# Optimization experiments

Hardware: AMD Instinct MI355X
Metric: run time of the kernel (lower is better)

## Reference

```python
import jax, jax.numpy as jnp
import numpy as np

H, HP, NH_M, NH_D = 1024, 64, 8, 8
B, T = 2, 2048
SPARSITY = 8
N_ROT = 32  # int(0.5 * HP), even
BASE = 10000.0


def _rope(x, pos, n_rot, base):
    # x: (..., L, d); pos: broadcastable to (..., L). Rotates first n_rot dims.
    half = n_rot // 2
    inv = base ** (-jnp.arange(half, dtype=x.dtype) / half)  # (half,)
    ang = pos[..., None] * inv                               # (..., L, half)
    cos, sin = jnp.cos(ang), jnp.sin(ang)
    x1, x2 = x[..., :half], x[..., half:n_rot]
    rot = jnp.concatenate([x1 * cos - x2 * sin, x1 * sin + x2 * cos], axis=-1)
    return jnp.concatenate([rot, x[..., n_rot:]], axis=-1)


def setup_inputs() -> dict:
    key = jax.random.key(0)
    ks = jax.random.split(key, 6)
    s = 0.02
    return {
        "X": jax.random.normal(ks[0], (B, T, H), jnp.float32),
        "mosa_router_w": jax.random.normal(ks[1], (H, NH_M), jnp.float32) * s,
        "mosa_wqkv": jax.random.normal(ks[2], (H, NH_M, 3 * HP), jnp.float32) * s,
        "mosa_wo": jax.random.normal(ks[3], (NH_M * HP, H), jnp.float32) * s,
        "dense_wqkv": jax.random.normal(ks[4], (H, NH_D, 3 * HP), jnp.float32) * s,
        "dense_wo": jax.random.normal(ks[5], (NH_D * HP, H), jnp.float32) * s,
    }


def _mosa_branch(X, router_w, wqkv, wo):
    # Expert-choice sparse attention: each head routes its own top-k tokens.
    b, t, _ = X.shape
    k = t // SPARSITY
    scores = jnp.einsum('bth,hn->bnt', X, router_w)                      # (b,nh,T)
    _, idx = jax.lax.top_k(scores, k)                                    # (b,nh,k)
    idx = jnp.sort(idx, axis=-1)                                         # keep temporal order
    gates = jax.nn.sigmoid(jnp.take_along_axis(scores, idx, axis=-1))    # (b,nh,k)
    Xg = jnp.take_along_axis(X[:, None], idx[..., None], axis=2)         # (b,nh,k,h)
    qkv = jnp.einsum('bnkh,hnd->bnkd', Xg, wqkv)                         # (b,nh,k,3hp)
    Q, K, V = jnp.split(qkv, 3, axis=-1)
    pos = idx.astype(X.dtype)                                            # original positions for RoPE
    Q = _rope(Q, pos, N_ROT, BASE)
    K = _rope(K, pos, N_ROT, BASE)
    att = jnp.einsum('bnqd,bnkd->bnqk', Q, K) / jnp.sqrt(jnp.asarray(HP, X.dtype))
    causal = idx[..., :, None] >= idx[..., None, :]                      # causality by original index
    att = jnp.where(causal, att, -jnp.inf)
    AV = jnp.einsum('bnqk,bnkd->bnqd', jax.nn.softmax(att, axis=-1), V)
    AV = AV * gates[..., None]
    # scatter selected-token outputs back to full sequence
    out = jnp.zeros((b, NH_M, t, HP), X.dtype)
    bi = jnp.arange(b)[:, None, None]
    hi = jnp.arange(NH_M)[None, :, None]
    out = out.at[bi, hi, idx].set(AV)                                    # (b,nh,T,hp)
    out = out.transpose(0, 2, 1, 3).reshape(b, t, NH_M * HP)
    return out @ wo


def _dense_branch(X, wqkv, wo):
    b, t, _ = X.shape
    qkv = jnp.einsum('bth,hnd->bntd', X, wqkv)                           # (b,nh,T,3hp)
    Q, K, V = jnp.split(qkv, 3, axis=-1)
    pos = jnp.arange(t, dtype=X.dtype)
    Q = _rope(Q, pos, N_ROT, BASE)
    K = _rope(K, pos, N_ROT, BASE)
    att = jnp.einsum('bnqd,bnkd->bnqk', Q, K) / jnp.sqrt(jnp.asarray(HP, X.dtype))
    causal = jnp.tril(jnp.ones((t, t), bool))
    att = jnp.where(causal, att, -jnp.inf)
    AV = jnp.einsum('bnqk,bnkd->bnqd', jax.nn.softmax(att, axis=-1), V)  # (b,nh,T,hp)
    return AV.transpose(0, 2, 1, 3).reshape(b, t, NH_D * HP) @ wo


def reference(X, mosa_router_w, mosa_wqkv, mosa_wo, dense_wqkv, dense_wo):
    return (_mosa_branch(X, mosa_router_w, mosa_wqkv, mosa_wo)
            + _dense_branch(X, dense_wqkv, dense_wo))
```

## Files before the change

kernel.cpp:

```cpp
#include <hip/hip_runtime.h>
#include <math.h>

constexpr int BB = 2;
constexpr int SEQ = 2048;
constexpr int HD = 1024;
constexpr int DH = 64;
constexpr int NHEAD = 8;
constexpr int D3 = 192;
constexpr int KSEL = 256;
constexpr float NEG = -1e30f;

typedef short short8 __attribute__((ext_vector_type(8)));
typedef float f32x4 __attribute__((ext_vector_type(4)));

__device__ __forceinline__ ushort bf16u(float f) {
  union { float f; unsigned u; } v; v.f = f;
  unsigned r = (v.u + 0x7FFFu + ((v.u >> 16) & 1u)) >> 16;
  return (ushort)r;
}
__device__ __forceinline__ float bf2f(ushort h) {
  union { unsigned u; float f; } v; v.u = ((unsigned)h) << 16;
  return v.f;
}

__device__ __forceinline__ void gl_lds16(const ushort* g, ushort* l) {
  __builtin_amdgcn_global_load_lds(
      (const __attribute__((address_space(1))) unsigned int*)g,
      (__attribute__((address_space(3))) unsigned int*)l, 16, 0, 0);
}

__device__ __forceinline__ unsigned long long rankkey(float s, int idx) {
  union { float f; unsigned u; } v; v.f = s;
  unsigned o = (v.u & 0x80000000u) ? ~v.u : (v.u | 0x80000000u);
  return ((unsigned long long)o << 11) | (unsigned)(2047 - idx);
}

__global__ void cast_bf16x4(const float* __restrict__ x, ushort* __restrict__ y, int n4) {
  int i = blockIdx.x * 256 + threadIdx.x;
  if (i >= n4) return;
  float4 v = ((const float4*)x)[i];
  ushort4 r; r.x = bf16u(v.x); r.y = bf16u(v.y); r.z = bf16u(v.z); r.w = bf16u(v.w);
  ((ushort4*)y)[i] = r;
}

__global__ __launch_bounds__(256) void transpose_cast2(
    const float* __restrict__ W1, ushort* __restrict__ T1,
    const float* __restrict__ W2, ushort* __restrict__ T2, int K, int N) {
  const float* W = blockIdx.z ? W2 : W1;
  ushort* Wt = blockIdx.z ? T2 : T1;
  __shared__ float tile[32][33];
  int n0 = blockIdx.x * 32, k0 = blockIdx.y * 32;
  int tx = threadIdx.x & 31, ty = threadIdx.x >> 5;
#pragma unroll
  for (int i = 0; i < 4; i++)
    tile[ty + 8 * i][tx] = W[(size_t)(k0 + ty + 8 * i) * N + n0 + tx];
  __syncthreads();
#pragma unroll
  for (int i = 0; i < 4; i++)
    Wt[(size_t)(n0 + ty + 8 * i) * K + k0 + tx] = bf16u(tile[tx][ty + 8 * i]);
}

__global__ __launch_bounds__(256) void router2(const float* __restrict__ X,
    const float* __restrict__ rw, float* __restrict__ scores) {
  __shared__ float rwT[8][8][132];
  int tid = threadIdx.x;
  for (int idx = tid; idx < 8192; idx += 256) {
    int h = idx & 1023, n = idx >> 10;
    rwT[n][h >> 7][h & 127] = rw[h * 8 + n];
  }
  __syncthreads();
  int row = blockIdx.x * 32 + (tid >> 3);
  int seg = tid & 7;
  const float* xrow = X + (size_t)row * HD + seg * 128;
  float acc[8] = {};
#pragma unroll 8
  for (int it = 0; it < 32; it++) {
    float4 xv = *(const float4*)(xrow + 4 * it);
#pragma unroll
    for (int n = 0; n < 8; n++) {
      float4 rv = *(const float4*)&rwT[n][seg][4 * it];
      acc[n] += xv.x * rv.x + xv.y * rv.y + xv.z * rv.z + xv.w * rv.w;
    }
  }
#pragma unroll
  for (int n = 0; n < 8; n++) {
    acc[n] += __shfl_xor(acc[n], 1);
    acc[n] += __shfl_xor(acc[n], 2);
    acc[n] += __shfl_xor(acc[n], 4);
  }
  int b = row >> 11, t2 = row & (SEQ - 1);
  scores[((size_t)b * NHEAD + seg) * SEQ + t2] = acc[seg];
}

__global__ __launch_bounds__(256) void topk_partial(const float* __restrict__ scores,
    int* __restrict__ pranks) {
  int row = blockIdx.x;
  int c = blockIdx.y;
  __shared__ unsigned long long ck[64];
  const float* sp = scores + (size_t)row * SEQ;
  int tid = threadIdx.x;
  if (tid < 64) ck[tid] = rankkey(sp[c * 64 + tid], c * 64 + tid);
  __syncthreads();
  unsigned long long kv[8]; int p[8];
#pragma unroll
  for (int i = 0; i < 8; i++) {
    int vi = i * 256 + tid;
    kv[i] = rankkey(sp[vi], vi);
    p[i] = 0;
  }
#pragma unroll 8
  for (int j = 0; j < 64; j += 2) {
    unsigned long long k0 = ck[j], k1 = ck[j + 1];
#pragma unroll
    for (int i = 0; i < 8; i++) {
      p[i] += (k0 > kv[i]);
      p[i] += (k1 > kv[i]);
    }
  }
#pragma unroll
  for (int i = 0; i < 8; i++)
    pranks[((size_t)row * 32 + c) * SEQ + i * 256 + tid] = p[i];
}

__global__ __launch_bounds__(1024) void topk_select(const float* __restrict__ scores,
    const int* __restrict__ pranks, int* __restrict__ sel, float* __restrict__ gates) {
  int bn = blockIdx.x;
  __shared__ int wsum[16];
  int tid = threadIdx.x;
  int t0 = tid * 2;
  int r0 = 0, r1 = 0;
#pragma unroll
  for (int c = 0; c < 32; c++) {
    const int2 pp = *(const int2*)&pranks[((size_t)bn * 32 + c) * SEQ + t0];
    r0 += pp.x; r1 += pp.y;
  }
  int f0 = r0 < KSEL, f1 = r1 < KSEL;
  unsigned long long b0 = __ballot(f0), b1 = __ballot(f1);
  int lane = tid & 63, wv = tid >> 6;
  unsigned long long lower = (1ULL << lane) - 1ULL;
  int before = __popcll(b0 & lower) + __popcll(b1 & lower);
  int wtotal = __popcll(b0) + __popcll(b1);
  if (lane == 0) wsum[wv] = wtotal;
  __syncthreads();
  int woff = 0;
#pragma unroll
  for (int i2 = 0; i2 < 16; i2++) woff += (i2 < wv) ? wsum[i2] : 0;
  int base = woff + before;
  if (f0) { sel[bn * KSEL + base] = t0;
            gates[bn * KSEL + base] = 1.f / (1.f + __expf(-scores[(size_t)bn * SEQ + t0]));
            base++; }
  if (f1) { sel[bn * KSEL + base] = t0 + 1;
            gates[bn * KSEL + base] = 1.f / (1.f + __expf(-scores[(size_t)bn * SEQ + t0 + 1])); }
}

__global__ __launch_bounds__(256) void gemm_mosa_bf16(const ushort* __restrict__ Xb,
    const ushort* __restrict__ Wt, const int* __restrict__ sel,
    ushort* __restrict__ Qmg, ushort* __restrict__ Kmg, ushort* __restrict__ Vtmg) {
  __shared__ __align__(16) ushort As[64][40];
  __shared__ __align__(16) ushort Bs[64][40];
  int bn = blockIdx.x; int b = bn >> 3, n = bn & 7;
  int m0 = blockIdx.y * 64, n0 = blockIdx.z * 64;
  int tid = threadIdx.x;
  int lane = tid & 63, w = tid >> 6;
  int wm = w & 1, wn = w >> 1;
  int cc = lane & 15, quad = lane >> 4;
  int sr = tid >> 2, sc4 = tid & 3;

  int grow = sel[bn * KSEL + m0 + sr];
  const ushort* arow = Xb + ((size_t)(b * SEQ) + grow) * HD;
  const ushort* brow = Wt + ((size_t)(n * D3 + n0 + sr)) * HD;

  f32x4 acc[2][2];
#pragma unroll
  for (int i = 0; i < 2; i++)
#pragma unroll
    for (int j = 0; j < 2; j++)
#pragma unroll
      for (int r = 0; r < 4; r++) acc[i][j][r] = 0.f;

  for (int k0 = 0; k0 < HD; k0 += 32) {
    __syncthreads();
    *(short8*)&As[sr][8 * sc4] = *(const short8*)(arow + k0 + 8 * sc4);
    *(short8*)&Bs[sr][8 * sc4] = *(const short8*)(brow + k0 + 8 * sc4);
    __syncthreads();
    short8 af[2], bf_[2];
#pragma unroll
    for (int i = 0; i < 2; i++) af[i] = *(const short8*)&As[32 * wm + 16 * i + cc][8 * quad];
#pragma unroll
    for (int j = 0; j < 2; j++) bf_[j] = *(const short8*)&Bs[32 * wn + 16 * j + cc][8 * quad];
#pragma unroll
    for (int i = 0; i < 2; i++)
#pragma unroll
      for (int j = 0; j < 2; j++)
        acc[i][j] = __builtin_amdgcn_mfma_f32_16x16x32_bf16(af[i], bf_[j], acc[i][j], 0, 0, 0);
  }

#pragma unroll
  for (int i = 0; i < 2; i++)
#pragma unroll
    for (int j = 0; j < 2; j++) {
      int col = n0 + 32 * wn + 16 * j + cc;
      int row0 = m0 + 32 * wm + 16 * i + 4 * quad;
      if (col < 64) {
#pragma unroll
        for (int r = 0; r < 4; r++)
          Qmg[((size_t)bn * KSEL + row0 + r) * 64 + col] = bf16u(acc[i][j][r] * 0.125f);
      } else if (col < 128) {
#pragma unroll
        for (int r = 0; r < 4; r++)
          Kmg[((size_t)bn * KSEL + row0 + r) * 64 + (col - 64)] = bf16u(acc[i][j][r]);
      } else {
        ushort4 pk;
        pk.x = bf16u(acc[i][j][0]); pk.y = bf16u(acc[i][j][1]);
        pk.z = bf16u(acc[i][j][2]); pk.w = bf16u(acc[i][j][3]);
        *(ushort4*)&Vtmg[((size_t)bn * 64 + (col - 128)) * KSEL + row0] = pk;
      }
    }
}

__global__ void rope_split(ushort* __restrict__ Qb, ushort* __restrict__ Kb,
                           const int* __restrict__ sel, int mosa) {
  int tid = blockIdx.x * 256 + threadIdx.x;
  int j = tid & 15;
  int which = (tid >> 4) & 1;
  int row = tid >> 5;
  float pos = mosa ? (float)sel[row] : (float)(row & (SEQ - 1));
  float inv = __expf((float)j * -0.5756462732485115f);
  float ang = pos * inv;
  float c = cosf(ang), sn = sinf(ang);
  ushort* p = (which ? Kb : Qb) + (size_t)row * 64 + j;
  float x1 = bf2f(p[0]), x2 = bf2f(p[16]);
  p[0] = bf16u(x1 * c - x2 * sn);
  p[16] = bf16u(x1 * sn + x2 * c);
}

__global__ __launch_bounds__(256) void flash5(
    const ushort* __restrict__ Qg, const ushort* __restrict__ Kg,
    const ushort* __restrict__ Vtg,
    const ushort* __restrict__ Qmg, const ushort* __restrict__ Kmg,
    const ushort* __restrict__ Vtmg,
    const int* __restrict__ sel, const float* __restrict__ gates,
    ushort* __restrict__ avd, ushort* __restrict__ avm) {
  __shared__ __align__(16) ushort Ks[2][64][64];
  __shared__ __align__(16) ushort Vt[2][64][64];
  __shared__ __align__(16) ushort Ps[64][64];

  int bx = blockIdx.x;
  bool mosa = bx >= 512;
  int bn, qt, T;
  const ushort *Qb, *Kb, *Vb;
  ushort* outp;
  if (!mosa) {
    bn = bx & 15;
    int pr = bx >> 4;
    qt = (pr < 16) ? (31 - pr) : (pr - 16);
    T = SEQ;
    Qb = Qg + (size_t)bn * SEQ * 64;
    Kb = Kg + (size_t)bn * SEQ * 64;
    Vb = Vtg + (size_t)bn * 64 * SEQ;
    outp = avd;
  } else {
    int rr = bx - 512;
    bn = rr & 15; qt = 3 - (rr >> 4); T = KSEL;
    Qb = Qmg + (size_t)bn * KSEL * 64;
    Kb = Kmg + (size_t)bn * KSEL * 64;
    Vb = Vtmg + (size_t)bn * 64 * KSEL;
    outp = avm;
  }
  int b = bn >> 3, n = bn & 7;
  int tid = threadIdx.x;
  int lane = tid & 63, w = tid >> 6;
  int cc = lane & 15, quad = lane >> 4;
  int qrow = 16 * w + cc;

  short8 bq[2];
  {
    const ushort* qsrc = Qb + (size_t)(qt * 64 + qrow) * 64;
    bq[0] = *(const short8*)(qsrc + 8 * quad);
    bq[1] = *(const short8*)(qsrc + 8 * (quad + 4));
  }

  int rloc = lane >> 3;
  int c_log = (lane & 7) ^ rloc;
  int row0 = 16 * w + rloc, row1 = row0 + 8;
  const ushort* pK0 = Kb + (size_t)row0 * 64 + 8 * c_log;
  const ushort* pK1 = Kb + (size_t)row1 * 64 + 8 * c_log;
  const ushort* pV0 = Vb + (size_t)row0 * T + 8 * c_log;
  const ushort* pV1 = Vb + (size_t)row1 * T + 8 * c_log;

  f32x4 oacc[4];
  float m = NEG, l = 0.f;
#pragma unroll
  for (int jd = 0; jd < 4; jd++)
#pragma unroll
    for (int r = 0; r < 4; r++) oacc[jd][r] = 0.f;

  gl_lds16(pK0, &Ks[0][16 * w][0]);
  gl_lds16(pK1, &Ks[0][16 * w + 8][0]);
  gl_lds16(pV0, &Vt[0][16 * w][0]);
  gl_lds16(pV1, &Vt[0][16 * w + 8][0]);

  for (int kt = 0; kt <= qt; kt++) {
    int buf = kt & 1;
    __syncthreads();
    if (kt < qt) {
      int nk = kt + 1, nb = buf ^ 1;
      gl_lds16(pK0 + (size_t)nk * 4096, &Ks[nb][16 * w][0]);
      gl_lds16(pK1 + (size_t)nk * 4096, &Ks[nb][16 * w + 8][0]);
      gl_lds16(pV0 + nk * 64, &Vt[nb][16 * w][0]);
      gl_lds16(pV1 + nk * 64, &Vt[nb][16 * w + 8][0]);
    }

    f32x4 sacc[4];
#pragma unroll
    for (int j = 0; j < 4; j++)
#pragma unroll
      for (int r = 0; r < 4; r++) sacc[j][r] = 0.f;
#pragma unroll
    for (int ks = 0; ks < 2; ks++) {
#pragma unroll
      for (int j = 0; j < 4; j++) {
        int krow = 16 * j + cc;
        short8 ak = *(const short8*)&Ks[buf][krow][8 * ((quad + 4 * ks) ^ (krow & 7))];
        sacc[j] = __builtin_amdgcn_mfma_f32_16x16x32_bf16(ak, bq[ks], sacc[j], 0, 0, 0);
      }
    }
    if (kt == qt) {
#pragma unroll
      for (int j = 0; j < 4; j++)
#pragma unroll
        for (int r = 0; r < 4; r++)
          if (16 * j + 4 * quad + r > qrow) sacc[j][r] = NEG;
    }
    float mx = NEG;
#pragma unroll
    for (int j = 0; j < 4; j++)
#pragma unroll
      for (int r = 0; r < 4; r++) mx = fmaxf(mx, sacc[j][r]);
    mx = fmaxf(mx, __shfl_xor(mx, 16));
    mx = fmaxf(mx, __shfl_xor(mx, 32));
    float mn = fmaxf(m, mx);
    float sc = __expf(m - mn);
    m = mn;
    float rsum = 0.f;
    float p[4][4];
#pragma unroll
    for (int j = 0; j < 4; j++)
#pragma unroll
      for (int r = 0; r < 4; r++) { p[j][r] = __expf(sacc[j][r] - mn); rsum += p[j][r]; }
    rsum += __shfl_xor(rsum, 16);
    rsum += __shfl_xor(rsum, 32);
    l = l * sc + rsum;
#pragma unroll
    for (int j = 0; j < 4; j++) {
      ushort4 pk;
      pk.x = bf16u(p[j][0]); pk.y = bf16u(p[j][1]);
      pk.z = bf16u(p[j][2]); pk.w = bf16u(p[j][3]);
      int phys = (2 * j + (quad >> 1)) ^ (qrow & 7);
      *(ushort4*)&Ps[qrow][phys * 8 + 4 * (quad & 1)] = pk;
    }
#pragma unroll
    for (int r = 0; r < 4; r++) {
      float scr = __shfl(sc, 16 * quad + 4 * quad + r);
#pragma unroll
      for (int jd = 0; jd < 4; jd++) oacc[jd][r] *= scr;
    }
    __asm__ volatile("s_waitcnt lgkmcnt(0)" ::: "memory");
#pragma unroll
    for (int ks = 0; ks < 2; ks++) {
      short8 ap = *(const short8*)&Ps[qrow][8 * ((quad + 4 * ks) ^ (qrow & 7))];
#pragma unroll
      for (int jd = 0; jd < 4; jd++) {
        int vrow = 16 * jd + cc;
        short8 bv = *(const short8*)&Vt[buf][vrow][8 * ((quad + 4 * ks) ^ (vrow & 7))];
        oacc[jd] = __builtin_amdgcn_mfma_f32_16x16x32_bf16(ap, bv, oacc[jd], 0, 0, 0);
      }
    }
  }

#pragma unroll
  for (int r = 0; r < 4; r++) {
    float lr = __shfl(l, 16 * quad + 4 * quad + r);
    int q = qt * 64 + 16 * w + 4 * quad + r;
    float scale;
    size_t row;
    if (mosa) {
      int trow = sel[bn * KSEL + q];
      scale = gates[bn * KSEL + q] / lr;
      row = (size_t)(b * SEQ + trow);
    } else {
      scale = 1.f / lr;
      row = (size_t)(b * SEQ + q);
    }
    ushort* orow = outp + row * (NHEAD * DH) + n * DH;
#pragma unroll
    for (int jd = 0; jd < 4; jd++)
      orow[16 * jd + cc] = bf16u(oacc[jd][r] * scale);
  }
}

template <int MODE>
__global__ __launch_bounds__(256) void gemm_bf16(
    const ushort* __restrict__ A1, const ushort* __restrict__ B1t, int K1,
    const ushort* __restrict__ A2, const ushort* __restrict__ B2t, int K2,
    void* __restrict__ outv, int N,
    ushort* __restrict__ Qo, ushort* __restrict__ Ko, ushort* __restrict__ Vto) {
  __shared__ __align__(16) ushort As[128][32];
  __shared__ __align__(16) ushort Bs[128][32];
  int m0 = blockIdx.x * 128, n0 = blockIdx.y * 128;
  int tid = threadIdx.x;
  int lane = tid & 63, wave = tid >> 6;
  int wm = wave & 1, wn = wave >> 1;
  int cc = lane & 15, quad = lane >> 4;

  int srow = 16 * wave + (lane >> 2);
  int c_log = ((lane & 3) - (lane >> 3)) & 3;

  f32x4 acc[4][4];
#pragma unroll
  for (int i = 0; i < 4; i++)
#pragma unroll
    for (int j = 0; j < 4; j++)
#pragma unroll
      for (int r = 0; r < 4; r++) acc[i][j][r] = 0.f;

  const int npass = (MODE == 0) ? 2 : 1;
  for (int pass = 0; pass < npass; pass++) {
    const ushort* A = pass ? A2 : A1;
    const ushort* Bt = pass ? B2t : B1t;
    int K = pass ? K2 : K1;
    const ushort* pA0 = A + (size_t)(m0 + srow) * K + 8 * c_log;
    const ushort* pA1 = A + (size_t)(m0 + srow + 64) * K + 8 * c_log;
    const ushort* pB0 = Bt + (size_t)(n0 + srow) * K + 8 * c_log;
    const ushort* pB1 = Bt + (size_t)(n0 + srow + 64) * K + 8 * c_log;
    for (int k0 = 0; k0 < K; k0 += 32) {
      __syncthreads();
      gl_lds16(pA0 + k0, &As[16 * wave][0]);
      gl_lds16(pA1 + k0, &As[16 * wave + 64][0]);
      gl_lds16(pB0 + k0, &Bs[16 * wave][0]);
      gl_lds16(pB1 + k0, &Bs[16 * wave + 64][0]);
      __syncthreads();
      short8 af[4], bfr[4];
#pragma unroll
      for (int i = 0; i < 4; i++) {
        int ra = 64 * wm + 16 * i + cc;
        af[i] = *(const short8*)&As[ra][8 * ((quad + (ra >> 1)) & 3)];
      }
#pragma unroll
      for (int j = 0; j < 4; j++) {
        int rb = 64 * wn + 16 * j + cc;
        bfr[j] = *(const short8*)&Bs[rb][8 * ((quad + (rb >> 1)) & 3)];
      }
#pragma unroll
      for (int i = 0; i < 4; i++)
#pragma unroll
        for (int j = 0; j < 4; j++)
          acc[i][j] = __builtin_amdgcn_mfma_f32_16x16x32_bf16(af[i], bfr[j], acc[i][j], 0, 0, 0);
    }
  }

#pragma unroll
  for (int i = 0; i < 4; i++) {
#pragma unroll
    for (int j = 0; j < 4; j++) {
      int colg = n0 + 64 * wn + 16 * j + cc;
      int row0 = m0 + 64 * wm + 16 * i + 4 * quad;
      if (MODE == 0) {
#pragma unroll
        for (int r = 0; r < 4; r++)
          ((float*)outv)[(size_t)(row0 + r) * N + colg] = acc[i][j][r];
      } else {
        int nn = colg / 192, c = colg % 192;
        int b2 = row0 >> 11, t2 = row0 & 2047;
        int bn2 = b2 * 8 + nn;
        if (c < 64) {
#pragma unroll
          for (int r = 0; r < 4; r++)
            Qo[((size_t)bn2 * SEQ + t2 + r) * 64 + c] = bf16u(acc[i][j][r] * 0.125f);
        } else if (c < 128) {
#pragma unroll
          for (int r = 0; r < 4; r++)
            Ko[((size_t)bn2 * SEQ + t2 + r) * 64 + (c - 64)] = bf16u(acc[i][j][r]);
        } else {
          ushort4 pk;
          pk.x = bf16u(acc[i][j][0]); pk.y = bf16u(acc[i][j][1]);
          pk.z = bf16u(acc[i][j][2]); pk.w = bf16u(acc[i][j][3]);
          *(ushort4*)&Vto[((size_t)bn2 * 64 + (c - 128)) * SEQ + t2] = pk;
        }
      }
    }
  }
}

extern "C" void kernel_launch(void* const* d_in, const int* in_sizes, int n_in,
                              void* d_out, int out_size, void* d_ws, size_t ws_size,
                              hipStream_t stream) {
  const float* X          = (const float*)d_in[0];
  const float* router_w   = (const float*)d_in[1];
  const float* mosa_wqkv  = (const float*)d_in[2];
  const float* mosa_wo    = (const float*)d_in[3];
  const float* dense_wqkv = (const float*)d_in[4];
  const float* dense_wo   = (const float*)d_in[5];
  float* out = (float*)d_out;
  char* ws = (char*)d_ws;

  float*  scores  = (float*) (ws + 0);
  int*    sel     = (int*)   (ws + 131072);
  float*  gates   = (float*) (ws + 147456);
  ushort* avm     = (ushort*)(ws + 163840);
  ushort* avd     = (ushort*)(ws + 4358144);
  ushort* Xb      = (ushort*)(ws + 8552448);
  ushort* Wqkv_t  = (ushort*)(ws + 16941056);
  ushort* Wmq_t   = (ushort*)(ws + 20086784);
  ushort* Wdo_t   = (ushort*)(ws + 23232512);
  ushort* Wmo_t   = (ushort*)(ws + 24281088);
  ushort* Qg      = (ushort*)(ws + 25329664);
  ushort* Kg      = (ushort*)(ws + 29523968);
  ushort* Vtg     = (ushort*)(ws + 33718272);
  ushort* Qmg     = (ushort*)(ws + 37912576);
  ushort* Kmg     = (ushort*)(ws + 38436864);
  ushort* Vtmg    = (ushort*)(ws + 38961152);
  int*    pranks  = (int*)   (ws + 39485440);

  hipMemsetAsync(avm, 0, (size_t)BB * SEQ * NHEAD * DH * sizeof(ushort), stream);

  cast_bf16x4<<<4096, 256, 0, stream>>>(X, Xb, BB * SEQ * HD / 4);
  transpose_cast2<<<dim3(48, 32, 2), 256, 0, stream>>>(dense_wqkv, Wqkv_t,
                                                       mosa_wqkv, Wmq_t, 1024, 1536);
  transpose_cast2<<<dim3(32, 16, 2), 256, 0, stream>>>(dense_wo, Wdo_t,
                                                       mosa_wo, Wmo_t, 512, 1024);

  router2<<<BB * SEQ / 32, 256, 0, stream>>>(X, router_w, scores);
  topk_partial<<<dim3(BB * NHEAD, 32), 256, 0, stream>>>(scores, pranks);
  topk_select<<<BB * NHEAD, 1024, 0, stream>>>(scores, pranks, sel, gates);

  gemm_mosa_bf16<<<dim3(BB * NHEAD, KSEL / 64, D3 / 64), 256, 0, stream>>>(
      Xb, Wmq_t, sel, Qmg, Kmg, Vtmg);
  rope_split<<<(BB * NHEAD * KSEL * 32) / 256, 256, 0, stream>>>(Qmg, Kmg, sel, 1);
  gemm_bf16<1><<<dim3(32, 12), 256, 0, stream>>>(Xb, Wqkv_t, 1024,
      (const ushort*)nullptr, (const ushort*)nullptr, 0, nullptr, NHEAD * D3,
      Qg, Kg, Vtg);
  rope_split<<<(BB * NHEAD * SEQ * 32) / 256, 256, 0, stream>>>(Qg, Kg, nullptr, 0);

  flash5<<<576, 256, 0, stream>>>(Qg, Kg, Vtg, Qmg, Kmg, Vtmg, sel, gates, avd, avm);

  gemm_bf16<0><<<dim3(32, 8), 256, 0, stream>>>(avm, Wmo_t, 512, avd, Wdo_t, 512, out, HD,
                                                nullptr, nullptr, nullptr);
}
```

Measured before the change: 234.6 us.

## Split dense causal attention KV range across four blocks with merge kernel

The dense-branch flash kernel now splits each query tile's causal KV loop into four interleaved strides (kstart, step 4), launching 2048 dense blocks instead of 512. Each block writes unnormalized bf16 partial outputs plus per-row (max, sum) to a workspace. A new flash_merge kernel combines the four partials with log-sum-exp weights. The aim is to fix the load imbalance of the causal triangle and give the GPU more parallelism. The cost is an extra launch, roughly 16 MB of extra partial-output traffic, and bf16 rounding of the unnormalized partials.

```diff
diff --git a/kernel.cpp b/kernel.cpp
--- a/kernel.cpp
+++ b/kernel.cpp
@@ -234,38 +234,35 @@
   p[16] = bf16u(x1 * sn + x2 * c);
 }
 
-__global__ __launch_bounds__(256) void flash5(
+__global__ __launch_bounds__(256) void flash6(
     const ushort* __restrict__ Qg, const ushort* __restrict__ Kg,
     const ushort* __restrict__ Vtg,
     const ushort* __restrict__ Qmg, const ushort* __restrict__ Kmg,
     const ushort* __restrict__ Vtmg,
     const int* __restrict__ sel, const float* __restrict__ gates,
-    ushort* __restrict__ avd, ushort* __restrict__ avm) {
+    ushort* __restrict__ Opart, float2* __restrict__ Mlp,
+    ushort* __restrict__ avm) {
   __shared__ __align__(16) ushort Ks[2][64][64];
   __shared__ __align__(16) ushort Vt[2][64][64];
   __shared__ __align__(16) ushort Ps[64][64];
 
   int bx = blockIdx.x;
-  bool mosa = bx >= 512;
-  int bn, qt, T;
+  bool mosa = bx >= 2048;
+  int bn, qt, T, kstart, kstride;
   const ushort *Qb, *Kb, *Vb;
-  ushort* outp;
   if (!mosa) {
-    bn = bx & 15;
-    int pr = bx >> 4;
-    qt = (pr < 16) ? (31 - pr) : (pr - 16);
-    T = SEQ;
+    bn = bx & 15; qt = (bx >> 4) & 31;
+    kstart = bx >> 9; kstride = 4; T = SEQ;
     Qb = Qg + (size_t)bn * SEQ * 64;
     Kb = Kg + (size_t)bn * SEQ * 64;
     Vb = Vtg + (size_t)bn * 64 * SEQ;
-    outp = avd;
   } else {
-    int rr = bx - 512;
-    bn = rr & 15; qt = 3 - (rr >> 4); T = KSEL;
+    int rr = bx - 2048;
+    bn = rr & 15; qt = 3 - (rr >> 4);
+    kstart = 0; kstride = 1; T = KSEL;
     Qb = Qmg + (size_t)bn * KSEL * 64;
     Kb = Kmg + (size_t)bn * KSEL * 64;
     Vb = Vtmg + (size_t)bn * 64 * KSEL;
-    outp = avm;
   }
   int b = bn >> 3, n = bn & 7;
   int tid = threadIdx.x;
@@ -295,16 +292,20 @@
 #pragma unroll
     for (int r = 0; r < 4; r++) oacc[jd][r] = 0.f;
 
-  gl_lds16(pK0, &Ks[0][16 * w][0]);
-  gl_lds16(pK1, &Ks[0][16 * w + 8][0]);
-  gl_lds16(pV0, &Vt[0][16 * w][0]);
-  gl_lds16(pV1, &Vt[0][16 * w + 8][0]);
-
-  for (int kt = 0; kt <= qt; kt++) {
-    int buf = kt & 1;
+  if (kstart <= qt) {
+    gl_lds16(pK0 + (size_t)kstart * 4096, &Ks[0][16 * w][0]);
+    gl_lds16(pK1 + (size_t)kstart * 4096, &Ks[0][16 * w + 8][0]);
+    gl_lds16(pV0 + kstart * 64, &Vt[0][16 * w][0]);
+    gl_lds16(pV1 + kstart * 64, &Vt[0][16 * w + 8][0]);
+  }
+
+  int it = 0;
+  for (int kt = kstart; kt <= qt; kt += kstride, it++) {
+    int buf = it & 1;
     __syncthreads();
-    if (kt < qt) {
-      int nk = kt + 1, nb = buf ^ 1;
+    int nk = kt + kstride;
+    if (nk <= qt) {
+      int nb = buf ^ 1;
       gl_lds16(pK0 + (size_t)nk * 4096, &Ks[nb][16 * w][0]);
       gl_lds16(pK1 + (size_t)nk * 4096, &Ks[nb][16 * w + 8][0]);
       gl_lds16(pV0 + nk * 64, &Vt[nb][16 * w][0]);
@@ -378,25 +379,59 @@
     }
   }
 
-#pragma unroll
-  for (int r = 0; r < 4; r++) {
-    float lr = __shfl(l, 16 * quad + 4 * quad + r);
-    int q = qt * 64 + 16 * w + 4 * quad + r;
-    float scale;
-    size_t row;
-    if (mosa) {
+  if (!mosa) {
+    size_t pb = ((size_t)(bn * 32 + qt) * 4 + (size_t)(kstart));
+    ushort* obase = Opart + pb * 4096;
+#pragma unroll
+    for (int r = 0; r < 4; r++) {
+      int ql = 16 * w + 4 * quad + r;
+#pragma unroll
+      for (int jd = 0; jd < 4; jd++)
+        obase[ql * 64 + 16 * jd + cc] = bf16u(oacc[jd][r]);
+    }
+    if (quad == 0) Mlp[pb * 64 + qrow] = make_float2(m, l);
+  } else {
+#pragma unroll
+    for (int r = 0; r < 4; r++) {
+      float lr = __shfl(l, 16 * quad + 4 * quad + r);
+      int q = qt * 64 + 16 * w + 4 * quad + r;
       int trow = sel[bn * KSEL + q];
-      scale = gates[bn * KSEL + q] / lr;
-      row = (size_t)(b * SEQ + trow);
-    } else {
-      scale = 1.f / lr;
-      row = (size_t)(b * SEQ + q);
-    }
-    ushort* orow = outp + row * (NHEAD * DH) + n * DH;
-#pragma unroll
-    for (int jd = 0; jd < 4; jd++)
-      orow[16 * jd + cc] = bf16u(oacc[jd][r] * scale);
-  }
+      float scale = gates[bn * KSEL + q] / lr;
+      size_t row = (size_t)(b * SEQ + trow);
+      ushort* orow = avm + row * (NHEAD * DH) + n * DH;
+#pragma unroll
+      for (int jd = 0; jd < 4; jd++)
+        orow[16 * jd + cc] = bf16u(oacc[jd][r] * scale);
+    }
+  }
+}
+
+__global__ __launch_bounds__(256) void flash_merge(const ushort* __restrict__ Opart,
+    const float2* __restrict__ Mlp, ushort* __restrict__ avd) {
+  int bq = blockIdx.x;
+  int bn = bq >> 5, qt = bq & 31;
+  int b = bn >> 3, n = bn & 7;
+  int tid = threadIdx.x;
+  int q = tid >> 2, ds = (tid & 3) * 16;
+  size_t pb = (size_t)bq * 4;
+  float2 ml[4];
+#pragma unroll
+  for (int c = 0; c < 4; c++) ml[c] = Mlp[(pb + c) * 64 + q];
+  float M = fmaxf(fmaxf(ml[0].x, ml[1].x), fmaxf(ml[2].x, ml[3].x));
+  float wgt[4], L = 0.f;
+#pragma unroll
+  for (int c = 0; c < 4; c++) { wgt[c] = __expf(ml[c].x - M); L += wgt[c] * ml[c].y; }
+  float inv = 1.f / L;
+  float acc[16] = {};
+#pragma unroll
+  for (int c = 0; c < 4; c++) {
+    const ushort* op = Opart + (pb + c) * 4096 + q * 64 + ds;
+#pragma unroll
+    for (int d = 0; d < 16; d++) acc[d] += wgt[c] * bf2f(op[d]);
+  }
+  ushort* orow = avd + ((size_t)(b * SEQ + qt * 64 + q)) * (NHEAD * DH) + n * DH + ds;
+#pragma unroll
+  for (int d = 0; d < 16; d++) orow[d] = bf16u(acc[d] * inv);
 }
 
 template <int MODE>
@@ -521,6 +556,8 @@
   ushort* Kmg     = (ushort*)(ws + 38436864);
   ushort* Vtmg    = (ushort*)(ws + 38961152);
   int*    pranks  = (int*)   (ws + 39485440);
+  ushort* Opart   = (ushort*)(ws + 43679744);
+  float2* Mlp     = (float2*)(ws + 60456960);
 
   hipMemsetAsync(avm, 0, (size_t)BB * SEQ * NHEAD * DH * sizeof(ushort), stream);
 
@@ -542,7 +579,9 @@
       Qg, Kg, Vtg);
   rope_split<<<(BB * NHEAD * SEQ * 32) / 256, 256, 0, stream>>>(Qg, Kg, nullptr, 0);
 
-  flash5<<<576, 256, 0, stream>>>(Qg, Kg, Vtg, Qmg, Kmg, Vtmg, sel, gates, avd, avm);
+  flash6<<<2112, 256, 0, stream>>>(Qg, Kg, Vtg, Qmg, Kmg, Vtmg, sel, gates,
+                                   Opart, Mlp, avm);
+  flash_merge<<<512, 256, 0, stream>>>(Opart, Mlp, avd);
 
   gemm_bf16<0><<<dim3(32, 8), 256, 0, stream>>>(avm, Wmo_t, 512, avd, Wdo_t, 512, out, HD,
                                                 nullptr, nullptr, nullptr);
```

Result: faster. 224.8 us (-4.2%).
